# Performance work log

Hardware: AMD Instinct MI355X
Metric: run time of the kernel (lower is better)

Reference implementation:

```python
import jax, jax.numpy as jnp
import numpy as np

EPS = 1e-6
HOPS = 3


def setup_inputs() -> dict:
    key = jax.random.key(0)
    ks = jax.random.split(key, 10)
    NA = NB = 50000
    E = 625000
    D = 128
    xA = jax.random.normal(ks[0], (NA, D), dtype=jnp.float32)
    xB = jax.random.normal(ks[1], (NB, D), dtype=jnp.float32)
    attAB = jax.random.uniform(ks[2], (E,), dtype=jnp.float32)
    attBA = jax.random.uniform(ks[3], (E,), dtype=jnp.float32)
    # AlphaCalculation params (xavier-ish small init per gain=0.02)
    fc1_w = jax.random.normal(ks[4], (D, D), dtype=jnp.float32) * 0.02
    fc1_b = jnp.zeros((D,), dtype=jnp.float32)
    fc2_w = jax.random.normal(ks[5], (1, D), dtype=jnp.float32) * 0.02
    fc2_b = jnp.zeros((1,), dtype=jnp.float32)
    eAB = jax.random.randint(ks[6], (2, E), 0, NA)  # src in A, dst in B
    eBA = jax.random.randint(ks[7], (2, E), 0, NB)  # src in B, dst in A
    return {"xA": xA, "xB": xB, "attAB": attAB, "attBA": attBA,
            "fc1_w": fc1_w, "fc1_b": fc1_b, "fc2_w": fc2_w, "fc2_b": fc2_b,
            "eAB": eAB, "eBA": eBA}


def _aggregate(edge_index, src_feat_all, attention, num_dst):
    # gather -> scale -> scatter-add
    msg = src_feat_all[edge_index[0]] * attention[:, None]  # [E, D]
    return jax.ops.segment_sum(msg, edge_index[1], num_segments=num_dst)


def reference(xA, xB, attAB, attBA, fc1_w, fc1_b, fc2_w, fc2_b, eAB, eBA):
    NA, NB = xA.shape[0], xB.shape[0]
    feat0A, feat0B = xA, xB
    # global embedding: mean over node types of per-type mean -> [1, D]
    g = 0.5 * (xA.mean(axis=0, keepdims=True) + xB.mean(axis=0, keepdims=True))
    # alpha = sigmoid(fc2(tanh(fc1(g)))).squeeze(-1), clamped
    h = jnp.tanh(g @ fc1_w.T + fc1_b)
    alpha = jax.nn.sigmoid(h @ fc2_w.T + fc2_b).squeeze(-1)  # [1]
    alpha = jnp.clip(alpha, EPS, 1.0 - EPS)
    curA, curB = feat0A, feat0B
    for _ in range(HOPS):
        # dst A receives from B via eBA; dst B receives from A via eAB
        msgA = _aggregate(eBA, curB, attBA, NA)
        msgB = _aggregate(eAB, curA, attAB, NB)
        newA = jnp.clip(feat0A * alpha + msgA * (1.0 - alpha), EPS, 1.0 / EPS)
        newB = jnp.clip(feat0B * alpha + msgB * (1.0 - alpha), EPS, 1.0 / EPS)
        curA, curB = newA, newB
    # concat node types for a single output array [NA+NB, D]
    return jnp.concatenate([curA, curB], axis=0)
```

## Files before the change

### kernel.cpp

```cpp
#include <hip/hip_runtime.h>
#include <math.h>

#define D 128
#define EPSV 1e-6f
#define CLIP_HI 1e6f
#define G 512
#define SCAN_ELEMS 1024
#define HCF 128
#define SLOTS 48

typedef float v4f __attribute__((ext_vector_type(4)));

__device__ __forceinline__ unsigned short f2bf(float f) {
    unsigned u = __float_as_uint(f);
    u = u + 0x7FFFu + ((u >> 16) & 1u);
    return (unsigned short)(u >> 16);
}
__device__ __forceinline__ void fma8(uint4 u, float a, float* acc) {
    acc[0] += __uint_as_float(u.x << 16) * a;
    acc[1] += __uint_as_float(u.x & 0xffff0000u) * a;
    acc[2] += __uint_as_float(u.y << 16) * a;
    acc[3] += __uint_as_float(u.y & 0xffff0000u) * a;
    acc[4] += __uint_as_float(u.z << 16) * a;
    acc[5] += __uint_as_float(u.z & 0xffff0000u) * a;
    acc[6] += __uint_as_float(u.w << 16) * a;
    acc[7] += __uint_as_float(u.w & 0xffff0000u) * a;
}
__device__ __forceinline__ void unpack8(uint4 u, float* f) {
    f[0] = __uint_as_float(u.x << 16);
    f[1] = __uint_as_float(u.x & 0xffff0000u);
    f[2] = __uint_as_float(u.y << 16);
    f[3] = __uint_as_float(u.y & 0xffff0000u);
    f[4] = __uint_as_float(u.z << 16);
    f[5] = __uint_as_float(u.z & 0xffff0000u);
    f[6] = __uint_as_float(u.w << 16);
    f[7] = __uint_as_float(u.w & 0xffff0000u);
}
__device__ __forceinline__ float4 nt_load4f(const float* p) {
    v4f t = __builtin_nontemporal_load(reinterpret_cast<const v4f*>(p));
    return make_float4(t.x, t.y, t.z, t.w);
}
__device__ __forceinline__ void nt_store4f(float* p, float a, float b, float c, float d) {
    v4f t = {a, b, c, d};
    __builtin_nontemporal_store(t, reinterpret_cast<v4f*>(p));
}
__device__ __forceinline__ long long nt_load_ll(const void* p) {
    return __builtin_nontemporal_load(reinterpret_cast<const long long*>(p));
}

__global__ __launch_bounds__(256) void colsum_bf16(
        const float* __restrict__ xA, const float* __restrict__ xB,
        int NA, int NB, float* __restrict__ partA, float* __restrict__ partB,
        unsigned short* __restrict__ tblA, unsigned short* __restrict__ tblB) {
    __shared__ float4 sh[256];
    int tid = threadIdx.x;
    int c4  = tid & 31;
    int rs  = tid >> 5;
    float4 sa = make_float4(0.f, 0.f, 0.f, 0.f);
    float4 sb = make_float4(0.f, 0.f, 0.f, 0.f);
    for (int r = blockIdx.x * 8 + rs; r < NA; r += gridDim.x * 8) {
        float4 v = *reinterpret_cast<const float4*>(xA + (size_t)r * D + c4 * 4);
        sa.x += v.x; sa.y += v.y; sa.z += v.z; sa.w += v.w;
        ushort4 o; o.x = f2bf(v.x); o.y = f2bf(v.y); o.z = f2bf(v.z); o.w = f2bf(v.w);
        *reinterpret_cast<ushort4*>(tblA + (size_t)r * D + c4 * 4) = o;
    }
    for (int r = blockIdx.x * 8 + rs; r < NB; r += gridDim.x * 8) {
        float4 v = *reinterpret_cast<const float4*>(xB + (size_t)r * D + c4 * 4);
        sb.x += v.x; sb.y += v.y; sb.z += v.z; sb.w += v.w;
        ushort4 o; o.x = f2bf(v.x); o.y = f2bf(v.y); o.z = f2bf(v.z); o.w = f2bf(v.w);
        *reinterpret_cast<ushort4*>(tblB + (size_t)r * D + c4 * 4) = o;
    }
    sh[tid] = sa; __syncthreads();
    if (tid < 128) { sh[tid].x += sh[tid+128].x; sh[tid].y += sh[tid+128].y; sh[tid].z += sh[tid+128].z; sh[tid].w += sh[tid+128].w; } __syncthreads();
    if (tid < 64)  { sh[tid].x += sh[tid+64].x;  sh[tid].y += sh[tid+64].y;  sh[tid].z += sh[tid+64].z;  sh[tid].w += sh[tid+64].w;  } __syncthreads();
    if (tid < 32)  {
        float4 t = sh[tid]; float4 u = sh[tid+32];
        t.x += u.x; t.y += u.y; t.z += u.z; t.w += u.w;
        *reinterpret_cast<float4*>(partA + (size_t)blockIdx.x * D + tid * 4) = t;
    }
    __syncthreads();
    sh[tid] = sb; __syncthreads();
    if (tid < 128) { sh[tid].x += sh[tid+128].x; sh[tid].y += sh[tid+128].y; sh[tid].z += sh[tid+128].z; sh[tid].w += sh[tid+128].w; } __syncthreads();
    if (tid < 64)  { sh[tid].x += sh[tid+64].x;  sh[tid].y += sh[tid+64].y;  sh[tid].z += sh[tid+64].z;  sh[tid].w += sh[tid+64].w;  } __syncthreads();
    if (tid < 32)  {
        float4 t = sh[tid]; float4 u = sh[tid+32];
        t.x += u.x; t.y += u.y; t.z += u.z; t.w += u.w;
        *reinterpret_cast<float4*>(partB + (size_t)blockIdx.x * D + tid * 4) = t;
    }
}

__global__ __launch_bounds__(1024) void compute_alpha(
        const float* __restrict__ partA, const float* __restrict__ partB,
        int NA, int NB,
        const float* __restrict__ fc1_w, const float* __restrict__ fc1_b,
        const float* __restrict__ fc2_w, const float* __restrict__ fc2_b,
        float* __restrict__ alpha_out) {
    __shared__ float redA[1024];
    __shared__ float redB[1024];
    __shared__ float g[D];
    __shared__ float h[D];
    int tid = threadIdx.x;
    int c = tid & 127;
    int slice = tid >> 7;
    float sa = 0.f, sb = 0.f;
    for (int b = slice; b < G; b += 8) {
        sa += partA[(size_t)b * D + c];
        sb += partB[(size_t)b * D + c];
    }
    redA[tid] = sa; redB[tid] = sb;
    __syncthreads();
    if (tid < 512) { redA[tid] += redA[tid + 512]; redB[tid] += redB[tid + 512]; } __syncthreads();
    if (tid < 256) { redA[tid] += redA[tid + 256]; redB[tid] += redB[tid + 256]; } __syncthreads();
    if (tid < 128) {
        float ta = redA[tid] + redA[tid + 128];
        float tb = redB[tid] + redB[tid + 128];
        g[c] = 0.5f * (ta / (float)NA + tb / (float)NB);
    }
    __syncthreads();
    if (tid < 128) {
        float acc = fc1_b[c];
        for (int k = 0; k < D; ++k) acc += g[k] * fc1_w[(size_t)c * D + k];
        h[c] = tanhf(acc);
    }
    __syncthreads();
    if (tid == 0) {
        float a = fc2_b[0];
        for (int k = 0; k < D; ++k) a += h[k] * fc2_w[k];
        a = 1.f / (1.f + expf(-a));
        a = fminf(fmaxf(a, EPSV), 1.f - EPSV);
        *alpha_out = a;
    }
}

__global__ __launch_bounds__(256) void hist_dst2(
        const int* __restrict__ eA, int E, int* __restrict__ countsA,
        const int* __restrict__ eB, int* __restrict__ countsB) {
    int t = blockIdx.x * blockDim.x + threadIdx.x;
    if (t < E) {
        int dst = __builtin_nontemporal_load(&eA[E + t]);
        atomicAdd(&countsA[dst], 1);
    } else {
        int e = t - E;
        if (e < E) {
            int dst = __builtin_nontemporal_load(&eB[E + e]);
            atomicAdd(&countsB[dst], 1);
        }
    }
}

__global__ void scan_p1(const int* __restrict__ cA, int NAe, int nbA, int* __restrict__ bsA,
                        const int* __restrict__ cB, int NBe, int* __restrict__ bsB) {
    const int* c; int N; int* bs; int b;
    if ((int)blockIdx.x < nbA) { c = cA; N = NAe; bs = bsA; b = blockIdx.x; }
    else                       { c = cB; N = NBe; bs = bsB; b = blockIdx.x - nbA; }
    __shared__ int red[256];
    int tid = threadIdx.x;
    int base = b * SCAN_ELEMS + tid * 4;
    int s = 0;
    #pragma unroll
    for (int i = 0; i < 4; ++i) { int idx = base + i; if (idx < N) s += c[idx]; }
    red[tid] = s;
    __syncthreads();
    for (int off = 128; off > 0; off >>= 1) {
        if (tid < off) red[tid] += red[tid + off];
        __syncthreads();
    }
    if (tid == 0) bs[b] = red[0];
}

__global__ void scan_p2(int* __restrict__ bsA, int nbA, int* __restrict__ rpA, int NAe,
                        int* __restrict__ bsB, int nbB, int* __restrict__ rpB, int NBe) {
    int* bs; int nb; int* rp; int N;
    if (blockIdx.x == 0) { bs = bsA; nb = nbA; rp = rpA; N = NAe; }
    else                 { bs = bsB; nb = nbB; rp = rpB; N = NBe; }
    if (threadIdx.x == 0) {
        int run = 0;
        for (int i = 0; i < nb; ++i) { int t = bs[i]; bs[i] = run; run += t; }
        rp[N] = run;
    }
}

__global__ void scan_p3(int* __restrict__ cA, int NAe, const int* __restrict__ bsA, int nbA,
                        int* __restrict__ rpA,
                        int* __restrict__ cB, int NBe, const int* __restrict__ bsB,
                        int* __restrict__ rpB) {
    int* c; int N; const int* bs; int* rp; int b;
    if ((int)blockIdx.x < nbA) { c = cA; N = NAe; bs = bsA; rp = rpA; b = blockIdx.x; }
    else                       { c = cB; N = NBe; bs = bsB; rp = rpB; b = blockIdx.x - nbA; }
    __shared__ int sh[256];
    int tid = threadIdx.x;
    int base = b * SCAN_ELEMS + tid * 4;
    int v[4]; int s = 0;
    #pragma unroll
    for (int i = 0; i < 4; ++i) { int idx = base + i; v[i] = (idx < N) ? c[idx] : 0; s += v[i]; }
    sh[tid] = s;
    __syncthreads();
    for (int off = 1; off < 256; off <<= 1) {
        int t = (tid >= off) ? sh[tid - off] : 0;
        __syncthreads();
        sh[tid] += t;
        __syncthreads();
    }
    int excl = bs[b] + sh[tid] - s;
    #pragma unroll
    for (int i = 0; i < 4; ++i) {
        int idx = base + i;
        if (idx < N) { rp[idx] = excl; c[idx] = excl; excl += v[i]; }
    }
}

__global__ __launch_bounds__(256) void fill_part(
        const int* __restrict__ eA, const float* __restrict__ attA,
        int* __restrict__ curA, int2* __restrict__ entA, int NA,
        const int* __restrict__ eB, const float* __restrict__ attB,
        int* __restrict__ curB, int2* __restrict__ entB, int NB, int E, int slots) {
    int b = blockIdx.x;
    int combo = b & 15;
    int dir   = combo >> 3;
    int range = combo & 7;
    int chunk = b >> 4;
    const int* e; const float* att; int* cur; int2* ent; int N;
    if (dir == 0) { e = eA; att = attA; cur = curA; ent = entA; N = NA; }
    else          { e = eB; att = attB; cur = curB; ent = entB; N = NB; }
    int lo = (int)((long)range * N >> 3), hi = (int)((long)(range + 1) * N >> 3);
    for (int i = chunk * 256 + threadIdx.x; i < E; i += HCF * 256) {
        int dst = __builtin_nontemporal_load(&e[E + i]);
        if (dst >= lo && dst < hi) {
            int pos = atomicAdd(&cur[dst], 1);
            size_t idx; bool ok;
            if (slots) { ok = pos < slots; idx = (size_t)dst * slots + pos; }
            else       { ok = true;        idx = (size_t)pos; }
            if (ok) {
                int2 v;
                v.x = __builtin_nontemporal_load(&e[i]);
                v.y = __float_as_int(__builtin_nontemporal_load(&att[i]));
                ent[idx] = v;
            }
        }
    }
}

template <int LAST>
__global__ __launch_bounds__(256) void aggregate4(
        const int* __restrict__ dgA, const int2* __restrict__ entA,
        const unsigned short* __restrict__ gtA, const unsigned short* __restrict__ fxA,
        const float* __restrict__ fx32A,
        unsigned short* __restrict__ obfA, float* __restrict__ of32A, int NA, int nblkA,
        const int* __restrict__ dgB, const int2* __restrict__ entB,
        const unsigned short* __restrict__ gtB, const unsigned short* __restrict__ fxB,
        const float* __restrict__ fx32B,
        unsigned short* __restrict__ obfB, float* __restrict__ of32B, int NB,
        const float* __restrict__ alpha_p, int fx32on, int slots) {
    int b = blockIdx.x;
    int wid = threadIdx.x >> 6;
    int lane = threadIdx.x & 63;
    int g = lane >> 4;
    int l = lane & 15;
    const int* dg; const int2* entbase; const unsigned short* gt; const unsigned short* fx;
    const float* fx32; unsigned short* obf; float* of32; int N; int row;
    if (b < nblkA) {
        dg = dgA; entbase = entA; gt = gtA; fx = fxA; fx32 = fx32A;
        obf = obfA; of32 = of32A; N = NA;
        row = b * 4 + wid;
    } else {
        dg = dgB; entbase = entB; gt = gtB; fx = fxB; fx32 = fx32B;
        obf = obfB; of32 = of32B; N = NB;
        row = (b - nblkA) * 4 + wid;
    }
    if (row >= N) return;
    size_t base; int deg;
    if (slots) {
        base = (size_t)row * slots;
        int c = dg[row];
        deg = c < slots ? c : slots;
    } else {
        int b0 = dg[row];
        base = (size_t)b0;
        deg = dg[row + 1] - b0;
    }
    const int2* ent = entbase + base;
    float acc[8] = {0.f, 0.f, 0.f, 0.f, 0.f, 0.f, 0.f, 0.f};
    int off = l * 8;
    int j = 0;
    for (; j + 7 < deg; j += 8) {
        long long r0 = nt_load_ll(&ent[j + g]);
        long long r1 = nt_load_ll(&ent[j + 4 + g]);
        uint4 u0 = *reinterpret_cast<const uint4*>(gt + ((size_t)(unsigned)r0) * D + off);
        uint4 u1 = *reinterpret_cast<const uint4*>(gt + ((size_t)(unsigned)r1) * D + off);
        fma8(u0, __int_as_float((int)(r0 >> 32)), acc);
        fma8(u1, __int_as_float((int)(r1 >> 32)), acc);
    }
    for (; j < deg; j += 4) {
        int je = j + g;
        if (je < deg) {
            long long r0 = nt_load_ll(&ent[je]);
            uint4 u0 = *reinterpret_cast<const uint4*>(gt + ((size_t)(unsigned)r0) * D + off);
            fma8(u0, __int_as_float((int)(r0 >> 32)), acc);
        }
    }
    #pragma unroll
    for (int k = 0; k < 8; ++k) {
        acc[k] += __shfl_xor(acc[k], 16);
        acc[k] += __shfl_xor(acc[k], 32);
    }
    if (g == 0) {
        float al = alpha_p[0], bl = 1.f - al;
        float fv[8];
        if (fx32on) {
            float4 f0v = nt_load4f(fx32 + (size_t)row * D + off);
            float4 f1v = nt_load4f(fx32 + (size_t)row * D + off + 4);
            fv[0] = f0v.x; fv[1] = f0v.y; fv[2] = f0v.z; fv[3] = f0v.w;
            fv[4] = f1v.x; fv[5] = f1v.y; fv[6] = f1v.z; fv[7] = f1v.w;
        } else {
            uint4 f = *reinterpret_cast<const uint4*>(fx + (size_t)row * D + off);
            unpack8(f, fv);
        }
        float r[8];
        #pragma unroll
        for (int k = 0; k < 8; ++k)
            r[k] = fminf(fmaxf(fv[k] * al + acc[k] * bl, EPSV), CLIP_HI);
        if (LAST) {
            nt_store4f(of32 + (size_t)row * D + off,     r[0], r[1], r[2], r[3]);
            nt_store4f(of32 + (size_t)row * D + off + 4, r[4], r[5], r[6], r[7]);
        } else {
            uint4 o;
            o.x = (unsigned)f2bf(r[0]) | ((unsigned)f2bf(r[1]) << 16);
            o.y = (unsigned)f2bf(r[2]) | ((unsigned)f2bf(r[3]) << 16);
            o.z = (unsigned)f2bf(r[4]) | ((unsigned)f2bf(r[5]) << 16);
            o.w = (unsigned)f2bf(r[6]) | ((unsigned)f2bf(r[7]) << 16);
            *reinterpret_cast<uint4*>(obf + (size_t)row * D + off) = o;
        }
    }
}

__global__ void scatter_add(const float* __restrict__ cur, const float* __restrict__ att,
                            const int* __restrict__ edges, int E,
                            float* __restrict__ msg) {
    const long long total = (long long)E * (D / 4);
    long long stride = (long long)gridDim.x * blockDim.x;
    for (long long idx = (long long)blockIdx.x * blockDim.x + threadIdx.x;
         idx < total; idx += stride) {
        int e  = (int)(idx >> 5);
        int ch = (int)(idx & 31);
        int src = edges[e];
        int dst = edges[E + e];
        float a = att[e];
        const float4 v = *reinterpret_cast<const float4*>(cur + (size_t)src * D + ch * 4);
        float* p = msg + (size_t)dst * D + ch * 4;
        atomicAdd(p + 0, v.x * a);
        atomicAdd(p + 1, v.y * a);
        atomicAdd(p + 2, v.z * a);
        atomicAdd(p + 3, v.w * a);
    }
}

__global__ void combine(const float4* __restrict__ feat0, const float4* __restrict__ msg,
                        const float* __restrict__ alpha_p, float4* __restrict__ out, int n4) {
    float a = alpha_p[0];
    float b = 1.f - a;
    int stride = gridDim.x * blockDim.x;
    for (int i = blockIdx.x * blockDim.x + threadIdx.x; i < n4; i += stride) {
        float4 f = feat0[i];
        float4 m = msg[i];
        float4 r;
        r.x = fminf(fmaxf(f.x * a + m.x * b, EPSV), CLIP_HI);
        r.y = fminf(fmaxf(f.y * a + m.y * b, EPSV), CLIP_HI);
        r.z = fminf(fmaxf(f.z * a + m.z * b, EPSV), CLIP_HI);
        r.w = fminf(fmaxf(f.w * a + m.w * b, EPSV), CLIP_HI);
        out[i] = r;
    }
}

extern "C" void kernel_launch(void* const* d_in, const int* in_sizes, int n_in,
                              void* d_out, int out_size, void* d_ws, size_t ws_size,
                              hipStream_t stream) {
    const float* xA    = (const float*)d_in[0];
    const float* xB    = (const float*)d_in[1];
    const float* attAB = (const float*)d_in[2];
    const float* attBA = (const float*)d_in[3];
    const float* fc1_w = (const float*)d_in[4];
    const float* fc1_b = (const float*)d_in[5];
    const float* fc2_w = (const float*)d_in[6];
    const float* fc2_b = (const float*)d_in[7];
    const int*   eAB   = (const int*)d_in[8];
    const int*   eBA   = (const int*)d_in[9];

    const int NA = in_sizes[0] / D;
    const int NB = in_sizes[1] / D;
    const int E  = in_sizes[2];

    float* out  = (float*)d_out;
    float* outA = out;
    float* outB = out + (size_t)NA * D;

    const size_t TBL = (size_t)(NA + NB) * D;

    {
        unsigned short* tblP = (unsigned short*)d_ws;
        unsigned short* tblQ = tblP + TBL;
        unsigned short* xtab = tblQ + TBL;
        int2*  ellA  = (int2*)(xtab + TBL);
        int2*  ellB  = ellA + (size_t)NA * SLOTS;
        int*   cntA  = (int*)(ellB + (size_t)NB * SLOTS);
        int*   cntB  = cntA + NA;
        float* partA = (float*)(cntB + NB);
        float* partB = partA + (size_t)G * D;
        float* alpha = partB + (size_t)G * D;
        size_t needed1 = (size_t)((char*)(alpha + 4) - (char*)d_ws);

        if (ws_size >= needed1) {
            unsigned short* xtabA = xtab, *xtabB = xtab + (size_t)NA * D;
            unsigned short* tblPA = tblP, *tblPB = tblP + (size_t)NA * D;
            unsigned short* tblQA = tblQ, *tblQB = tblQ + (size_t)NA * D;

            colsum_bf16<<<G, 256, 0, stream>>>(xA, xB, NA, NB, partA, partB, xtabA, xtabB);
            compute_alpha<<<1, 1024, 0, stream>>>(partA, partB, NA, NB,
                                                  fc1_w, fc1_b, fc2_w, fc2_b, alpha);

            hipMemsetAsync(cntA, 0, (size_t)(NA + NB) * sizeof(int), stream);
            fill_part<<<16 * HCF, 256, 0, stream>>>(eBA, attBA, cntA, ellA, NA,
                                                    eAB, attAB, cntB, ellB, NB, E, SLOTS);

            int gA = (NA + 3) / 4, gB = (NB + 3) / 4;
            aggregate4<0><<<gA + gB, 256, 0, stream>>>(
                cntA, ellA, xtabB, xtabA, xA, tblPA, nullptr, NA, gA,
                cntB, ellB, xtabA, xtabB, xB, tblPB, nullptr, NB, alpha, 0, SLOTS);
            aggregate4<0><<<gA + gB, 256, 0, stream>>>(
                cntA, ellA, tblPB, xtabA, xA, tblQA, nullptr, NA, gA,
                cntB, ellB, tblPA, xtabB, xB, tblQB, nullptr, NB, alpha, 0, SLOTS);
            aggregate4<1><<<gA + gB, 256, 0, stream>>>(
                cntA, ellA, tblQB, xtabA, xA, nullptr, outA, NA, gA,
                cntB, ellB, tblQA, xtabB, xB, nullptr, outB, NB, alpha, 0, SLOTS);
            return;
        }
    }

    {
        unsigned short* tblP = (unsigned short*)d_ws;
        unsigned short* tblQ = tblP + TBL;
        int2*  csrA   = (int2*)(tblQ + TBL);
        int2*  csrB   = csrA + E;
        float* partA  = (float*)(csrB + E);
        float* partB  = partA + (size_t)G * D;
        float* alpha  = partB + (size_t)G * D;
        int*   row_ptrA = (int*)(alpha + 4);
        int*   cursorA  = row_ptrA + (NA + 1);
        int*   row_ptrB = cursorA + NA;
        int*   cursorB  = row_ptrB + (NB + 1);
        int*   bsA      = cursorB + NB;
        int*   bsB      = bsA + 64;
        unsigned short* tblX = (unsigned short*)(bsB + 64);
        size_t needed2 = (size_t)((char*)tblX - (char*)d_ws);
        size_t needed3 = needed2 + TBL * sizeof(unsigned short);

        if (ws_size >= needed2) {
            const int use3 = (ws_size >= needed3) ? 1 : 0;
            unsigned short* xtab  = use3 ? tblX : tblQ;
            unsigned short* xtabA = xtab, *xtabB = xtab + (size_t)NA * D;
            unsigned short* tblPA = tblP, *tblPB = tblP + (size_t)NA * D;
            unsigned short* tblQA = tblQ, *tblQB = tblQ + (size_t)NA * D;

            colsum_bf16<<<G, 256, 0, stream>>>(xA, xB, NA, NB, partA, partB, xtabA, xtabB);
            compute_alpha<<<1, 1024, 0, stream>>>(partA, partB, NA, NB,
                                                  fc1_w, fc1_b, fc2_w, fc2_b, alpha);

            hipMemsetAsync(cursorA, 0, (size_t)NA * sizeof(int), stream);
            hipMemsetAsync(cursorB, 0, (size_t)NB * sizeof(int), stream);
            int hb2 = (2 * E + 255) / 256;
            hist_dst2<<<hb2, 256, 0, stream>>>(eBA, E, cursorA, eAB, cursorB);

            int nbA = (NA + SCAN_ELEMS - 1) / SCAN_ELEMS;
            int nbB = (NB + SCAN_ELEMS - 1) / SCAN_ELEMS;
            scan_p1<<<nbA + nbB, 256, 0, stream>>>(cursorA, NA, nbA, bsA, cursorB, NB, bsB);
            scan_p2<<<2, 64, 0, stream>>>(bsA, nbA, row_ptrA, NA, bsB, nbB, row_ptrB, NB);
            scan_p3<<<nbA + nbB, 256, 0, stream>>>(cursorA, NA, bsA, nbA, row_ptrA,
                                                   cursorB, NB, bsB, row_ptrB);

            fill_part<<<16 * HCF, 256, 0, stream>>>(eBA, attBA, cursorA, csrA, NA,
                                                    eAB, attAB, cursorB, csrB, NB, E, 0);

            int gA = (NA + 3) / 4, gB = (NB + 3) / 4;
            int fx32on = use3 ? 0 : 1;
            aggregate4<0><<<gA + gB, 256, 0, stream>>>(
                row_ptrA, csrA, xtabB, xtabA, xA, tblPA, nullptr, NA, gA,
                row_ptrB, csrB, xtabA, xtabB, xB, tblPB, nullptr, NB, alpha, fx32on, 0);
            aggregate4<0><<<gA + gB, 256, 0, stream>>>(
                row_ptrA, csrA, tblPB, xtabA, xA, tblQA, nullptr, NA, gA,
                row_ptrB, csrB, tblPA, xtabB, xB, tblQB, nullptr, NB, alpha, fx32on, 0);
            aggregate4<1><<<gA + gB, 256, 0, stream>>>(
                row_ptrA, csrA, tblQB, xtabA, xA, nullptr, outA, NA, gA,
                row_ptrB, csrB, tblQA, xtabB, xB, nullptr, outB, NB, alpha, fx32on, 0);
            return;
        }
    }

    {
        float* msgA  = (float*)d_ws;
        float* msgB  = msgA + (size_t)NA * D;
        float* pA    = msgB + (size_t)NB * D;
        float* pB    = pA + (size_t)G * D;
        float* alph  = pB + (size_t)G * D;

        colsum_bf16<<<G, 256, 0, stream>>>(xA, xB, NA, NB, pA, pB,
                                           (unsigned short*)msgA, (unsigned short*)msgB);
        compute_alpha<<<1, 1024, 0, stream>>>(pA, pB, NA, NB,
                                              fc1_w, fc1_b, fc2_w, fc2_b, alph);

        const size_t msgBytes = ((size_t)NA + (size_t)NB) * D * sizeof(float);
        for (int hop = 0; hop < 3; ++hop) {
            hipMemsetAsync(msgA, 0, msgBytes, stream);
            const float* fA = (hop == 0) ? xA : outA;
            const float* fB = (hop == 0) ? xB : outB;
            scatter_add<<<4096, 256, 0, stream>>>(fB, attBA, eBA, E, msgA);
            scatter_add<<<4096, 256, 0, stream>>>(fA, attAB, eAB, E, msgB);
            combine<<<2048, 256, 0, stream>>>((const float4*)xA, (const float4*)msgA,
                                              alph, (float4*)outA, NA * D / 4);
            combine<<<2048, 256, 0, stream>>>((const float4*)xB, (const float4*)msgB,
                                              alph, (float4*)outB, NB * D / 4);
        }
    }
}
```

Before: 288.4 us.

## Add ELL-specialized aggregate kernel, vectorize fill_part dst loads, nontemporal colsum loads

Adds aggregate5, which handles the fixed-slot ELL layout. It processes 16 slots per iteration with predicated loads, so four gathers per thread are in flight before any FMAs run. This replaces the generic aggregate4 on the ELL path, and aggregate4 keeps only the CSR branch. fill_part now reads destination indices four at a time as int4 vectors, with a tail loop that handles the leftover edges. colsum uses nontemporal loads for the input features. Masked slots gather row 0 with weight zero, which wastes some bandwidth on low-degree rows in exchange for more memory-level parallelism.

```diff
diff --git a/kernel.cpp b/kernel.cpp
--- a/kernel.cpp
+++ b/kernel.cpp
@@ -10,6 +10,7 @@
 #define SLOTS 48
 
 typedef float v4f __attribute__((ext_vector_type(4)));
+typedef int   v4i __attribute__((ext_vector_type(4)));
 
 __device__ __forceinline__ unsigned short f2bf(float f) {
     unsigned u = __float_as_uint(f);
@@ -46,6 +47,9 @@
 }
 __device__ __forceinline__ long long nt_load_ll(const void* p) {
     return __builtin_nontemporal_load(reinterpret_cast<const long long*>(p));
+}
+__device__ __forceinline__ v4i nt_load4i(const int* p) {
+    return __builtin_nontemporal_load(reinterpret_cast<const v4i*>(p));
 }
 
 __global__ __launch_bounds__(256) void colsum_bf16(
@@ -59,13 +63,13 @@
     float4 sa = make_float4(0.f, 0.f, 0.f, 0.f);
     float4 sb = make_float4(0.f, 0.f, 0.f, 0.f);
     for (int r = blockIdx.x * 8 + rs; r < NA; r += gridDim.x * 8) {
-        float4 v = *reinterpret_cast<const float4*>(xA + (size_t)r * D + c4 * 4);
+        float4 v = nt_load4f(xA + (size_t)r * D + c4 * 4);
         sa.x += v.x; sa.y += v.y; sa.z += v.z; sa.w += v.w;
         ushort4 o; o.x = f2bf(v.x); o.y = f2bf(v.y); o.z = f2bf(v.z); o.w = f2bf(v.w);
         *reinterpret_cast<ushort4*>(tblA + (size_t)r * D + c4 * 4) = o;
     }
     for (int r = blockIdx.x * 8 + rs; r < NB; r += gridDim.x * 8) {
-        float4 v = *reinterpret_cast<const float4*>(xB + (size_t)r * D + c4 * 4);
+        float4 v = nt_load4f(xB + (size_t)r * D + c4 * 4);
         sb.x += v.x; sb.y += v.y; sb.z += v.z; sb.w += v.w;
         ushort4 o; o.x = f2bf(v.x); o.y = f2bf(v.y); o.z = f2bf(v.z); o.w = f2bf(v.w);
         *reinterpret_cast<ushort4*>(tblB + (size_t)r * D + c4 * 4) = o;
@@ -223,19 +227,120 @@
     if (dir == 0) { e = eA; att = attA; cur = curA; ent = entA; N = NA; }
     else          { e = eB; att = attB; cur = curB; ent = entB; N = NB; }
     int lo = (int)((long)range * N >> 3), hi = (int)((long)(range + 1) * N >> 3);
-    for (int i = chunk * 256 + threadIdx.x; i < E; i += HCF * 256) {
-        int dst = __builtin_nontemporal_load(&e[E + i]);
-        if (dst >= lo && dst < hi) {
-            int pos = atomicAdd(&cur[dst], 1);
-            size_t idx; bool ok;
-            if (slots) { ok = pos < slots; idx = (size_t)dst * slots + pos; }
-            else       { ok = true;        idx = (size_t)pos; }
-            if (ok) {
-                int2 v;
-                v.x = __builtin_nontemporal_load(&e[i]);
-                v.y = __float_as_int(__builtin_nontemporal_load(&att[i]));
-                ent[idx] = v;
+    int E4 = E & ~3;
+    for (int i = (chunk * 256 + threadIdx.x) * 4; i < E4; i += HCF * 256 * 4) {
+        v4i d4 = nt_load4i(&e[E + i]);
+        #pragma unroll
+        for (int k = 0; k < 4; ++k) {
+            int dst = d4[k];
+            if (dst >= lo && dst < hi) {
+                int pos = atomicAdd(&cur[dst], 1);
+                size_t idx; bool ok;
+                if (slots) { ok = pos < slots; idx = (size_t)dst * slots + pos; }
+                else       { ok = true;        idx = (size_t)pos; }
+                if (ok) {
+                    int2 v;
+                    v.x = __builtin_nontemporal_load(&e[i + k]);
+                    v.y = __float_as_int(__builtin_nontemporal_load(&att[i + k]));
+                    ent[idx] = v;
+                }
             }
+        }
+    }
+    if (blockIdx.x == 0) {
+        for (int i = E4 + threadIdx.x; i < E; i += 256) {
+            int dst = e[E + i];
+            const int* curp = (dst >= lo && dst < hi) ? cur : nullptr;
+            if (dst >= lo && dst < hi) {
+                int pos = atomicAdd(&cur[dst], 1);
+                size_t idx; bool ok;
+                if (slots) { ok = pos < slots; idx = (size_t)dst * slots + pos; }
+                else       { ok = true;        idx = (size_t)pos; }
+                if (ok) { int2 v; v.x = e[i]; v.y = __float_as_int(att[i]); ent[idx] = v; }
+            }
+            (void)curp;
+        }
+    }
+}
+
+template <int LAST>
+__global__ __launch_bounds__(256) void aggregate5(
+        const int* __restrict__ cntA, const int2* __restrict__ ellA,
+        const unsigned short* __restrict__ gtA, const unsigned short* __restrict__ fxA,
+        unsigned short* __restrict__ obfA, float* __restrict__ of32A, int NA, int nblkA,
+        const int* __restrict__ cntB, const int2* __restrict__ ellB,
+        const unsigned short* __restrict__ gtB, const unsigned short* __restrict__ fxB,
+        unsigned short* __restrict__ obfB, float* __restrict__ of32B, int NB,
+        const float* __restrict__ alpha_p) {
+    int b = blockIdx.x;
+    int wid = threadIdx.x >> 6;
+    int lane = threadIdx.x & 63;
+    int g = lane >> 4;
+    int l = lane & 15;
+    const int* cnt; const int2* ellbase; const unsigned short* gt; const unsigned short* fx;
+    unsigned short* obf; float* of32; int N; int row;
+    if (b < nblkA) {
+        cnt = cntA; ellbase = ellA; gt = gtA; fx = fxA;
+        obf = obfA; of32 = of32A; N = NA;
+        row = b * 4 + wid;
+    } else {
+        cnt = cntB; ellbase = ellB; gt = gtB; fx = fxB;
+        obf = obfB; of32 = of32B; N = NB;
+        row = (b - nblkA) * 4 + wid;
+    }
+    if (row >= N) return;
+    int c = cnt[row];
+    int deg = c < SLOTS ? c : SLOTS;
+    const int2* ent = ellbase + (size_t)row * SLOTS;
+    float acc[8] = {0.f, 0.f, 0.f, 0.f, 0.f, 0.f, 0.f, 0.f};
+    int off = l * 8;
+
+#define PROC16(BASE)                                                          \
+    {                                                                         \
+        unsigned sv[4]; float av[4]; uint4 u[4];                              \
+        _Pragma("unroll")                                                     \
+        for (int k = 0; k < 4; ++k) {                                         \
+            int slot = (BASE) + k * 4 + g;                                    \
+            long long rr = nt_load_ll(&ent[slot]);                            \
+            bool valid = slot < deg;                                          \
+            sv[k] = valid ? (unsigned)rr : 0u;                                \
+            av[k] = valid ? __int_as_float((int)(rr >> 32)) : 0.0f;           \
+        }                                                                     \
+        _Pragma("unroll")                                                     \
+        for (int k = 0; k < 4; ++k)                                           \
+            u[k] = *reinterpret_cast<const uint4*>(gt + (size_t)sv[k] * D + off); \
+        _Pragma("unroll")                                                     \
+        for (int k = 0; k < 4; ++k) fma8(u[k], av[k], acc);                   \
+    }
+
+    PROC16(0);
+    for (int base = 16; base < deg; base += 16) PROC16(base);
+#undef PROC16
+
+    #pragma unroll
+    for (int k = 0; k < 8; ++k) {
+        acc[k] += __shfl_xor(acc[k], 16);
+        acc[k] += __shfl_xor(acc[k], 32);
+    }
+    if (g == 0) {
+        float al = alpha_p[0], bl = 1.f - al;
+        float fv[8];
+        uint4 f = *reinterpret_cast<const uint4*>(fx + (size_t)row * D + off);
+        unpack8(f, fv);
+        float r[8];
+        #pragma unroll
+        for (int k = 0; k < 8; ++k)
+            r[k] = fminf(fmaxf(fv[k] * al + acc[k] * bl, EPSV), CLIP_HI);
+        if (LAST) {
+            nt_store4f(of32 + (size_t)row * D + off,     r[0], r[1], r[2], r[3]);
+            nt_store4f(of32 + (size_t)row * D + off + 4, r[4], r[5], r[6], r[7]);
+        } else {
+            uint4 o;
+            o.x = (unsigned)f2bf(r[0]) | ((unsigned)f2bf(r[1]) << 16);
+            o.y = (unsigned)f2bf(r[2]) | ((unsigned)f2bf(r[3]) << 16);
+            o.z = (unsigned)f2bf(r[4]) | ((unsigned)f2bf(r[5]) << 16);
+            o.w = (unsigned)f2bf(r[6]) | ((unsigned)f2bf(r[7]) << 16);
+            *reinterpret_cast<uint4*>(obf + (size_t)row * D + off) = o;
         }
     }
 }
@@ -250,7 +355,7 @@
         const unsigned short* __restrict__ gtB, const unsigned short* __restrict__ fxB,
         const float* __restrict__ fx32B,
         unsigned short* __restrict__ obfB, float* __restrict__ of32B, int NB,
-        const float* __restrict__ alpha_p, int fx32on, int slots) {
+        const float* __restrict__ alpha_p, int fx32on) {
     int b = blockIdx.x;
     int wid = threadIdx.x >> 6;
     int lane = threadIdx.x & 63;
@@ -268,17 +373,9 @@
         row = (b - nblkA) * 4 + wid;
     }
     if (row >= N) return;
-    size_t base; int deg;
-    if (slots) {
-        base = (size_t)row * slots;
-        int c = dg[row];
-        deg = c < slots ? c : slots;
-    } else {
-        int b0 = dg[row];
-        base = (size_t)b0;
-        deg = dg[row + 1] - b0;
-    }
-    const int2* ent = entbase + base;
+    int b0 = dg[row];
+    int deg = dg[row + 1] - b0;
+    const int2* ent = entbase + (size_t)b0;
     float acc[8] = {0.f, 0.f, 0.f, 0.f, 0.f, 0.f, 0.f, 0.f};
     int off = l * 8;
     int j = 0;
@@ -422,15 +519,15 @@
                                                     eAB, attAB, cntB, ellB, NB, E, SLOTS);
 
             int gA = (NA + 3) / 4, gB = (NB + 3) / 4;
-            aggregate4<0><<<gA + gB, 256, 0, stream>>>(
-                cntA, ellA, xtabB, xtabA, xA, tblPA, nullptr, NA, gA,
-                cntB, ellB, xtabA, xtabB, xB, tblPB, nullptr, NB, alpha, 0, SLOTS);
-            aggregate4<0><<<gA + gB, 256, 0, stream>>>(
-                cntA, ellA, tblPB, xtabA, xA, tblQA, nullptr, NA, gA,
-                cntB, ellB, tblPA, xtabB, xB, tblQB, nullptr, NB, alpha, 0, SLOTS);
-            aggregate4<1><<<gA + gB, 256, 0, stream>>>(
-                cntA, ellA, tblQB, xtabA, xA, nullptr, outA, NA, gA,
-                cntB, ellB, tblQA, xtabB, xB, nullptr, outB, NB, alpha, 0, SLOTS);
+            aggregate5<0><<<gA + gB, 256, 0, stream>>>(
+                cntA, ellA, xtabB, xtabA, tblPA, nullptr, NA, gA,
+                cntB, ellB, xtabA, xtabB, tblPB, nullptr, NB, alpha);
+            aggregate5<0><<<gA + gB, 256, 0, stream>>>(
+                cntA, ellA, tblPB, xtabA, tblQA, nullptr, NA, gA,
+                cntB, ellB, tblPA, xtabB, tblQB, nullptr, NB, alpha);
+            aggregate5<1><<<gA + gB, 256, 0, stream>>>(
+                cntA, ellA, tblQB, xtabA, nullptr, outA, NA, gA,
+                cntB, ellB, tblQA, xtabB, nullptr, outB, NB, alpha);
             return;
         }
     }
@@ -483,13 +580,13 @@
             int fx32on = use3 ? 0 : 1;
             aggregate4<0><<<gA + gB, 256, 0, stream>>>(
                 row_ptrA, csrA, xtabB, xtabA, xA, tblPA, nullptr, NA, gA,
-                row_ptrB, csrB, xtabA, xtabB, xB, tblPB, nullptr, NB, alpha, fx32on, 0);
+                row_ptrB, csrB, xtabA, xtabB, xB, tblPB, nullptr, NB, alpha, fx32on);
             aggregate4<0><<<gA + gB, 256, 0, stream>>>(
                 row_ptrA, csrA, tblPB, xtabA, xA, tblQA, nullptr, NA, gA,
-                row_ptrB, csrB, tblPA, xtabB, xB, tblQB, nullptr, NB, alpha, fx32on, 0);
+                row_ptrB, csrB, tblPA, xtabB, xB, tblQB, nullptr, NB, alpha, fx32on);
             aggregate4<1><<<gA + gB, 256, 0, stream>>>(
                 row_ptrA, csrA, tblQB, xtabA, xA, nullptr, outA, NA, gA,
-                row_ptrB, csrB, tblQA, xtabB, xB, nullptr, outB, NB, alpha, fx32on, 0);
+                row_ptrB, csrB, tblQA, xtabB, xB, nullptr, outB, NB, alpha, fx32on);
             return;
         }
     }
```

Result: faster. 266.2 us (-7.7%).
